# Optimization experiments

Hardware: AMD Instinct MI355X
Metric: run time of the kernel (lower is better)

Reference implementation:

```python
import jax, jax.numpy as jnp
import numpy as np

N_NODES = 100000
N_EDGES = 800000
IN_DIM = 64
HID = 96
OUT_DIM = 1
N_LAYERS = 3
N_CENTRAL = 512
BN_EPS = 1e-5


def setup_inputs() -> dict:
    key = jax.random.key(0)
    ks = jax.random.split(key, 16)
    s = 0.1  # weight scale to keep activations tame
    return {
        "x": jax.random.normal(ks[0], (N_NODES, IN_DIM), jnp.float32),
        "edge_index": jax.random.randint(ks[1], (2, N_EDGES), 0, N_NODES, jnp.int64 if jax.config.jax_enable_x64 else jnp.int32),
        "batch": jnp.zeros((N_NODES,), jnp.int32),
        "central_node_idx": jax.random.randint(ks[2], (N_CENTRAL,), 0, N_NODES, jnp.int32),
        "W_emb": jax.random.normal(ks[3], (IN_DIM, HID), jnp.float32) * s,
        "b_emb": jax.random.normal(ks[4], (HID,), jnp.float32) * s,
        "conv_wl": jax.random.normal(ks[5], (N_LAYERS, HID, HID), jnp.float32) * s,
        "conv_bl": jax.random.normal(ks[6], (N_LAYERS, HID), jnp.float32) * s,
        "conv_wr": jax.random.normal(ks[7], (N_LAYERS, HID, HID), jnp.float32) * s,
        "bn_gamma": jnp.ones((N_LAYERS, HID), jnp.float32),
        "bn_beta": jnp.zeros((N_LAYERS, HID), jnp.float32),
        "W1": jax.random.normal(ks[8], (HID, HID), jnp.float32) * s,
        "b1": jax.random.normal(ks[9], (HID,), jnp.float32) * s,
        "W2": jax.random.normal(ks[10], (HID, OUT_DIM), jnp.float32) * s,
        "b2": jax.random.normal(ks[11], (OUT_DIM,), jnp.float32) * s,
    }


def _sage_mean_agg(h, src, dst, n):
    # PyG SAGEConv mean aggregation: mean of source features at each target node
    msg = h[src]                                             # [E, H] gather
    summed = jax.ops.segment_sum(msg, dst, num_segments=n)   # [N, H] scatter-add
    deg = jax.ops.segment_sum(jnp.ones((src.shape[0],), h.dtype), dst, num_segments=n)
    return summed / jnp.maximum(deg, 1.0)[:, None]


def reference(x, edge_index, batch, central_node_idx, W_emb, b_emb,
              conv_wl, conv_bl, conv_wr, bn_gamma, bn_beta, W1, b1, W2, b2):
    n = x.shape[0]
    src, dst = edge_index[0], edge_index[1]
    h = jax.nn.relu(x @ W_emb + b_emb)                       # [N, H]
    for i in range(conv_wl.shape[0]):
        agg = _sage_mean_agg(h, src, dst, n)
        # SAGEConv: lin_l(agg) (with bias) + lin_r(x_root) (no bias)
        h = agg @ conv_wl[i] + conv_bl[i] + h @ conv_wr[i]
        # BatchNorm1d, training mode: batch stats with biased variance
        mean = h.mean(axis=0)
        var = h.var(axis=0)
        h = (h - mean) * jax.lax.rsqrt(var + BN_EPS) * bn_gamma[i] + bn_beta[i]
        h = jax.nn.relu(h)
    central = h[central_node_idx]                            # [G, H]
    out = jax.nn.relu(central @ W1 + b1) @ W2 + b2           # [G, OUT]
    return out
```

## Files before the change

### kernel.cpp

```cpp
#include <hip/hip_runtime.h>

#define NN 100000
#define NE 800000
#define IND 64
#define HID 96
#define NL 3
#define NC 512
#define BN_EPS 1e-5f

#define NBE ((NN + 127) / 128)
#define NBP (NL * 9)
#define NBF ((NE + 4095) / 4096)
#define NBK2 196
#define BCAP 4864

typedef __attribute__((ext_vector_type(8))) short bf16x8;
typedef __attribute__((ext_vector_type(4))) float f32x4;

static __device__ __forceinline__ float b2f(ushort u) {
    union { uint i; float f; } v; v.i = ((uint)u) << 16; return v.f;
}
static __device__ __forceinline__ ushort f2b(float f) {
    union { float f; uint i; } v; v.f = f;
    uint r = v.i + 0x7FFFu + ((v.i >> 16) & 1u);
    return (ushort)(r >> 16);
}
static __device__ __forceinline__ uint pack2(float a, float b) {
    return (uint)f2b(a) | ((uint)f2b(b) << 16);
}

static __device__ __forceinline__ void prep_one(const float* srcA, const float* srcB,
                                                ushort* dst, int t) {
    int lane = t & 63;
    int ct = (t >> 6) % 6;
    int kt = t / (6 * 64);
    int k0 = kt * 32 + (lane >> 4) * 8;
    int col = ct * 16 + (lane & 15);
    ushort tmp[8];
#pragma unroll
    for (int j = 0; j < 8; ++j) {
        int k = k0 + j;
        const float* src = (srcB == nullptr || k < 96) ? srcA : srcB;
        int kk = (srcB == nullptr || k < 96) ? k : k - 96;
        tmp[j] = f2b(src[kk * HID + col]);
    }
    uint* od = (uint*)(dst + (size_t)t * 8);
    od[0] = (uint)tmp[0] | ((uint)tmp[1] << 16);
    od[1] = (uint)tmp[2] | ((uint)tmp[3] << 16);
    od[2] = (uint)tmp[4] | ((uint)tmp[5] << 16);
    od[3] = (uint)tmp[6] | ((uint)tmp[7] << 16);
}

__global__ __launch_bounds__(256) void k_front(const float* __restrict__ x,
        const float* __restrict__ W_emb, const float* __restrict__ bias,
        ushort* __restrict__ h,
        const float* __restrict__ conv_wl, const float* __restrict__ conv_wr,
        ushort* __restrict__ Bfl, float* __restrict__ stats,
        const int* __restrict__ ei, int* __restrict__ gcur,
        uint* __restrict__ part) {
    __shared__ __align__(16) char smem[24576];
    const int b = blockIdx.x;
    const int tid = threadIdx.x;
    if (b >= NBE) {
        if (b < NBE + NBP) {
            int idx = b - NBE;
            int l = idx / 9, bb = idx % 9;
            int t = bb * 256 + tid;
            if (t < 6 * 6 * 64)
                prep_one(conv_wl + (size_t)l * 9216, conv_wr + (size_t)l * 9216,
                         Bfl + (size_t)l * 18432, t);
            if (bb == 0 && tid < 192) stats[(size_t)l * 192 + tid] = 0.f;
        } else {
            uint* ordbuf = (uint*)smem;
            unsigned char* sbk = (unsigned char*)(smem + 16384);
            int* lhist = (int*)(smem + 20480);
            int* lscan = (int*)(smem + 21504);
            int* lbase = (int*)(smem + 22528);
            int* lcnt2 = (int*)(smem + 23552);
            const int base_e = (b - NBE - NBP) * 4096;
            lhist[tid] = 0; lcnt2[tid] = 0;
            __syncthreads();
#pragma unroll
            for (int it = 0; it < 16; ++it) {
                int e = base_e + it * 256 + tid;
                if (e < NE) atomicAdd(&lhist[ei[NE + e] >> 9], 1);
            }
            __syncthreads();
            int v = lhist[tid];
            lscan[tid] = v;
            __syncthreads();
            for (int off = 1; off < 256; off <<= 1) {
                int t2 = (tid >= off) ? lscan[tid - off] : 0;
                __syncthreads();
                lscan[tid] += t2;
                __syncthreads();
            }
            int excl = lscan[tid] - v;
            __syncthreads();
            lscan[tid] = excl;
            if (v > 0) lbase[tid] = atomicAdd(&gcur[tid], v);
            __syncthreads();
#pragma unroll
            for (int it = 0; it < 16; ++it) {
                int e = base_e + it * 256 + tid;
                if (e < NE) {
                    int s = ei[e], d = ei[NE + e];
                    int bk = d >> 9;
                    int lofs = atomicAdd(&lcnt2[bk], 1);
                    int slot = lscan[bk] + lofs;
                    ordbuf[slot] = (uint)s | ((uint)(d & 511) << 17);
                    sbk[slot] = (unsigned char)bk;
                }
            }
            __syncthreads();
            int total = NE - base_e; if (total > 4096) total = 4096;
            for (int i = tid; i < total; i += 256) {
                int bk = sbk[i];
                part[(size_t)bk * BCAP + lbase[bk] + (i - lscan[bk])] = ordbuf[i];
            }
        }
        return;
    }
    ushort* sB = (ushort*)smem;
    ushort* sT = (ushort*)smem;
    for (int i = tid; i < 768; i += 256) {
        int lane = i & 63;
        int ct = (i >> 6) % 6;
        int kt = i / (6 * 64);
        int k0 = kt * 32 + (lane >> 4) * 8;
        int col = ct * 16 + (lane & 15);
        ushort tmp[8];
#pragma unroll
        for (int j = 0; j < 8; ++j) tmp[j] = f2b(W_emb[(k0 + j) * HID + col]);
        uint4 o;
        o.x = (uint)tmp[0] | ((uint)tmp[1] << 16);
        o.y = (uint)tmp[2] | ((uint)tmp[3] << 16);
        o.z = (uint)tmp[4] | ((uint)tmp[5] << 16);
        o.w = (uint)tmp[6] | ((uint)tmp[7] << 16);
        ((uint4*)sB)[i] = o;
    }
    __syncthreads();
    const int wave = tid >> 6, lane = tid & 63;
    const int rowb = wave * 32;
    const int row0 = b * 128 + rowb;
    const int kof = (lane >> 4) * 8;
    f32x4 acc[2][6];
#pragma unroll
    for (int t = 0; t < 2; ++t)
#pragma unroll
        for (int c = 0; c < 6; ++c) acc[t][c] = (f32x4){0.f, 0.f, 0.f, 0.f};
#pragma unroll
    for (int kt = 0; kt < 2; ++kt) {
        int kk = kt * 32 + kof;
        bf16x8 a[2];
#pragma unroll
        for (int t = 0; t < 2; ++t) {
            int r = row0 + t * 16 + (lane & 15);
            if (r >= NN) r = NN - 1;
            const float* src = x + (size_t)r * IND + kk;
            float4 f0 = *(const float4*)src;
            float4 f1 = *(const float4*)(src + 4);
            a[t][0] = (short)f2b(f0.x); a[t][1] = (short)f2b(f0.y);
            a[t][2] = (short)f2b(f0.z); a[t][3] = (short)f2b(f0.w);
            a[t][4] = (short)f2b(f1.x); a[t][5] = (short)f2b(f1.y);
            a[t][6] = (short)f2b(f1.z); a[t][7] = (short)f2b(f1.w);
        }
#pragma unroll
        for (int ct = 0; ct < 6; ++ct) {
            bf16x8 bb = *(const bf16x8*)&sB[((kt * 6 + ct) * 64 + lane) * 8];
            acc[0][ct] = __builtin_amdgcn_mfma_f32_16x16x32_bf16(a[0], bb, acc[0][ct], 0, 0, 0);
            acc[1][ct] = __builtin_amdgcn_mfma_f32_16x16x32_bf16(a[1], bb, acc[1][ct], 0, 0, 0);
        }
    }
    __syncthreads();
#pragma unroll
    for (int t = 0; t < 2; ++t)
#pragma unroll
        for (int ct = 0; ct < 6; ++ct) {
            int col = ct * 16 + (lane & 15);
            float bv = bias[col];
#pragma unroll
            for (int i = 0; i < 4; ++i) {
                int rb = rowb + t * 16 + (lane >> 4) * 4 + i;
                float v = acc[t][ct][i] + bv;
                sT[rb * HID + col] = f2b(v > 0.f ? v : 0.f);
            }
        }
    __syncthreads();
    for (int i = tid; i < 1536; i += 256) {
        int r = i / 12;
        int g = b * 128 + r;
        if (g < NN) ((uint4*)(h + (size_t)g * HID))[i % 12] = ((uint4*)sT)[i];
    }
}

__global__ __launch_bounds__(256) void k_bscan(const int* __restrict__ gcur,
                                               int* __restrict__ bbase) {
    __shared__ int sd[256];
    const int tid = threadIdx.x;
    int v = (tid < NBK2) ? gcur[tid] : 0;
    sd[tid] = v;
    __syncthreads();
    for (int off = 1; off < 256; off <<= 1) {
        int t = (tid >= off) ? sd[tid - off] : 0;
        __syncthreads();
        sd[tid] += t;
        __syncthreads();
    }
    if (tid < NBK2) bbase[tid] = sd[tid] - v;
}

__global__ __launch_bounds__(256) void k_fill3(const uint* __restrict__ part,
        const int* __restrict__ gcur, const int* __restrict__ bbase,
        int* __restrict__ rp, int* __restrict__ col) {
    __shared__ int lh[512];
    __shared__ int lsc[512];
    __shared__ int pairs[256];
    const int tid = threadIdx.x;
    const int bk = blockIdx.x;
    lh[tid] = 0; lh[tid + 256] = 0;
    __syncthreads();
    const int cnt = gcur[bk];
    const uint* pb = part + (size_t)bk * BCAP;
    for (int e = tid; e < cnt; e += 256) atomicAdd(&lh[pb[e] >> 17], 1);
    __syncthreads();
    int p0 = lh[2 * tid], p1 = lh[2 * tid + 1];
    int ps = p0 + p1;
    pairs[tid] = ps;
    __syncthreads();
    for (int off = 1; off < 256; off <<= 1) {
        int t = (tid >= off) ? pairs[tid - off] : 0;
        __syncthreads();
        pairs[tid] += t;
        __syncthreads();
    }
    int base = bbase[bk];
    int excl = base + pairs[tid] - ps;
    lsc[2 * tid] = excl;
    lsc[2 * tid + 1] = excl + p0;
    __syncthreads();
    const int n0 = bk * 512;
    for (int i = tid; i < 512; i += 256) {
        int n = n0 + i;
        if (n < NN) rp[n] = lsc[i];
    }
    if (bk == NBK2 - 1 && tid == 0) rp[NN] = NE;
    __syncthreads();
    for (int e = tid; e < cnt; e += 256) {
        uint v = pb[e];
        int pos = atomicAdd(&lsc[v >> 17], 1);
        col[pos] = (int)(v & 0x1FFFF);
    }
}

__global__ __launch_bounds__(256, 8) void k_agg(const ushort* __restrict__ pre,
        const int* __restrict__ rp, const int* __restrict__ col,
        const float* __restrict__ stats, const float* __restrict__ gamma,
        const float* __restrict__ beta, ushort* __restrict__ agg) {
    __shared__ float sc[96], sh[96];
    const int tid = threadIdx.x;
    if (tid < 96) {
        float scv = 1.f, shv = 0.f;
        if (stats) {
            float mean = stats[tid] * (1.f / NN);
            float var  = stats[96 + tid] * (1.f / NN) - mean * mean;
            float s = gamma[tid] * rsqrtf(var + BN_EPS);
            scv = s; shv = beta[tid] - mean * s;
        }
        sc[tid] = scv; sh[tid] = shv;
    }
    __syncthreads();
    const int lane = tid & 15;
    const int n = blockIdx.x * 16 + (tid >> 4);
    if (n >= NN) return;
    const float s0a = sc[2*lane],      h0a = sh[2*lane];
    const float s0b = sc[2*lane + 1],  h0b = sh[2*lane + 1];
    const float s1a = sc[2*lane + 32], h1a = sh[2*lane + 32];
    const float s1b = sc[2*lane + 33], h1b = sh[2*lane + 33];
    const float s2a = sc[2*lane + 64], h2a = sh[2*lane + 64];
    const float s2b = sc[2*lane + 65], h2b = sh[2*lane + 65];
    const int e0 = rp[n], e1 = rp[n + 1];
    float a0 = 0.f, a1 = 0.f, a2 = 0.f, a3 = 0.f, a4 = 0.f, a5 = 0.f;
    const uint* hb = (const uint*)pre + lane;
    int e = e0;
    for (; e + 4 <= e1; e += 4) {
        uint u[4][3];
#pragma unroll
        for (int i = 0; i < 4; ++i) {
            const uint* r = hb + (size_t)col[e + i] * 48;
            u[i][0] = r[0]; u[i][1] = r[16]; u[i][2] = r[32];
        }
#pragma unroll
        for (int i = 0; i < 4; ++i) {
            a0 += fmaxf(b2f((ushort)u[i][0])         * s0a + h0a, 0.f);
            a1 += fmaxf(b2f((ushort)(u[i][0] >> 16)) * s0b + h0b, 0.f);
            a2 += fmaxf(b2f((ushort)u[i][1])         * s1a + h1a, 0.f);
            a3 += fmaxf(b2f((ushort)(u[i][1] >> 16)) * s1b + h1b, 0.f);
            a4 += fmaxf(b2f((ushort)u[i][2])         * s2a + h2a, 0.f);
            a5 += fmaxf(b2f((ushort)(u[i][2] >> 16)) * s2b + h2b, 0.f);
        }
    }
    for (; e < e1; ++e) {
        const uint* r = hb + (size_t)col[e] * 48;
        uint u0 = r[0], u1 = r[16], u2 = r[32];
        a0 += fmaxf(b2f((ushort)u0)         * s0a + h0a, 0.f);
        a1 += fmaxf(b2f((ushort)(u0 >> 16)) * s0b + h0b, 0.f);
        a2 += fmaxf(b2f((ushort)u1)         * s1a + h1a, 0.f);
        a3 += fmaxf(b2f((ushort)(u1 >> 16)) * s1b + h1b, 0.f);
        a4 += fmaxf(b2f((ushort)u2)         * s2a + h2a, 0.f);
        a5 += fmaxf(b2f((ushort)(u2 >> 16)) * s2b + h2b, 0.f);
    }
    int d = e1 - e0; if (d < 1) d = 1;
    float inv = 1.0f / (float)d;
    uint* ar = (uint*)agg + (size_t)n * 48 + lane;
    ar[0]  = pack2(a0 * inv, a1 * inv);
    ar[16] = pack2(a2 * inv, a3 * inv);
    ar[32] = pack2(a4 * inv, a5 * inv);
}

__global__ __launch_bounds__(256, 4) void k_gemm(const ushort* __restrict__ aggb,
        const ushort* __restrict__ pre, const ushort* __restrict__ Bf,
        const float* __restrict__ bl, ushort* __restrict__ hnew,
        float* __restrict__ stats,
        const float* __restrict__ statsP, const float* __restrict__ gammaP,
        const float* __restrict__ betaP) {
    __shared__ __align__(16) char smem[40704];
    ushort* sB = (ushort*)smem;
    ushort* sT = (ushort*)smem;
    float*  sredS = (float*)(smem + 36864);
    float*  sredQ = (float*)(smem + 38400);
    float2* sscsh = (float2*)(smem + 39936);
    const int tid = threadIdx.x;
    for (int i = tid; i < 2304; i += 256) ((uint4*)sB)[i] = ((const uint4*)Bf)[i];
    if (tid < 96) {
        float scv = 1.f, shv = 0.f;
        if (statsP) {
            float mean = statsP[tid] * (1.f / NN);
            float var  = statsP[96 + tid] * (1.f / NN) - mean * mean;
            float s = gammaP[tid] * rsqrtf(var + BN_EPS);
            scv = s; shv = betaP[tid] - mean * s;
        }
        sscsh[tid] = make_float2(scv, shv);
    }
    __syncthreads();
    const int wave = tid >> 6, lane = tid & 63;
    const int rowb = wave * 32;
    const int row0 = blockIdx.x * 128 + rowb;
    const int kof = (lane >> 4) * 8;
    f32x4 acc[2][6];
#pragma unroll
    for (int t = 0; t < 2; ++t)
#pragma unroll
        for (int c = 0; c < 6; ++c) acc[t][c] = (f32x4){0.f, 0.f, 0.f, 0.f};
#pragma unroll
    for (int kt = 0; kt < 6; ++kt) {
        bf16x8 a[2];
#pragma unroll
        for (int t = 0; t < 2; ++t) {
            int r = row0 + t * 16 + (lane & 15);
            if (r >= NN) r = NN - 1;
            if (kt < 3) {
                int kk = kt * 32 + kof;
                a[t] = *(const bf16x8*)(aggb + (size_t)r * HID + kk);
            } else {
                int kk = (kt - 3) * 32 + kof;
                bf16x8 raw = *(const bf16x8*)(pre + (size_t)r * HID + kk);
                union { bf16x8 h; uint u[4]; } pk;
#pragma unroll
                for (int j = 0; j < 4; ++j) {
                    float2 p0 = sscsh[kk + 2*j];
                    float2 p1 = sscsh[kk + 2*j + 1];
                    float v0 = fmaxf(b2f((ushort)raw[2*j])     * p0.x + p0.y, 0.f);
                    float v1 = fmaxf(b2f((ushort)raw[2*j + 1]) * p1.x + p1.y, 0.f);
                    pk.u[j] = pack2(v0, v1);
                }
                a[t] = pk.h;
            }
        }
#pragma unroll
        for (int ct = 0; ct < 6; ++ct) {
            bf16x8 bb = *(const bf16x8*)&sB[((kt * 6 + ct) * 64 + lane) * 8];
            acc[0][ct] = __builtin_amdgcn_mfma_f32_16x16x32_bf16(a[0], bb, acc[0][ct], 0, 0, 0);
            acc[1][ct] = __builtin_amdgcn_mfma_f32_16x16x32_bf16(a[1], bb, acc[1][ct], 0, 0, 0);
        }
    }
    __syncthreads();
    float s[6], q[6];
#pragma unroll
    for (int c = 0; c < 6; ++c) { s[c] = 0.f; q[c] = 0.f; }
#pragma unroll
    for (int t = 0; t < 2; ++t)
#pragma unroll
        for (int ct = 0; ct < 6; ++ct) {
            int col = ct * 16 + (lane & 15);
            float bv = bl[col];
#pragma unroll
            for (int i = 0; i < 4; ++i) {
                int rb = rowb + t * 16 + (lane >> 4) * 4 + i;
                int g = blockIdx.x * 128 + rb;
                float v = acc[t][ct][i] + bv;
                if (g < NN) { s[ct] += v; q[ct] += v * v; }
                sT[rb * HID + col] = f2b(v);
            }
        }
#pragma unroll
    for (int c = 0; c < 6; ++c) {
        s[c] += __shfl_xor(s[c], 16); s[c] += __shfl_xor(s[c], 32);
        q[c] += __shfl_xor(q[c], 16); q[c] += __shfl_xor(q[c], 32);
    }
    if (lane < 16) {
#pragma unroll
        for (int c = 0; c < 6; ++c) {
            sredS[wave * 96 + c * 16 + lane] = s[c];
            sredQ[wave * 96 + c * 16 + lane] = q[c];
        }
    }
    __syncthreads();
    if (tid < 96) {
        float S = sredS[tid] + sredS[96 + tid] + sredS[192 + tid] + sredS[288 + tid];
        float Q = sredQ[tid] + sredQ[96 + tid] + sredQ[192 + tid] + sredQ[288 + tid];
        atomicAdd(&stats[tid], S);
        atomicAdd(&stats[96 + tid], Q);
    }
    for (int i = tid; i < 1536; i += 256) {
        int r = i / 12;
        int g = blockIdx.x * 128 + r;
        if (g < NN) ((uint4*)(hnew + (size_t)g * HID))[i % 12] = ((uint4*)sT)[i];
    }
}

__global__ __launch_bounds__(128) void k_mlp(const ushort* __restrict__ pre,
        const int* __restrict__ cidx, const float* __restrict__ stats,
        const float* __restrict__ gamma, const float* __restrict__ beta,
        const float* __restrict__ W1, const float* __restrict__ b1,
        const float* __restrict__ W2, const float* __restrict__ b2,
        float* __restrict__ out) {
    __shared__ float nh[96];
    __shared__ float hid[96];
    __shared__ float red[128];
    const int c = blockIdx.x;
    const int node = cidx[c];
    const int tid = threadIdx.x;
    if (tid < 96) {
        float mean = stats[tid] * (1.f / NN);
        float var  = stats[96 + tid] * (1.f / NN) - mean * mean;
        float s = gamma[tid] * rsqrtf(var + BN_EPS);
        float v = b2f(pre[(size_t)node * 96 + tid]) * s + (beta[tid] - mean * s);
        nh[tid] = fmaxf(v, 0.f);
    }
    __syncthreads();
    if (tid < 96) {
        float a = 0.f;
        for (int k = 0; k < 96; ++k) a += nh[k] * W1[k * 96 + tid];
        hid[tid] = fmaxf(a + b1[tid], 0.f);
    }
    __syncthreads();
    red[tid] = (tid < 96) ? hid[tid] * W2[tid] : 0.f;
    __syncthreads();
    for (int off = 64; off > 0; off >>= 1) {
        if (tid < off) red[tid] += red[tid + off];
        __syncthreads();
    }
    if (tid == 0) out[c] = red[0] + b2[0];
}

extern "C" void kernel_launch(void* const* d_in, const int* in_sizes, int n_in,
                              void* d_out, int out_size, void* d_ws, size_t ws_size,
                              hipStream_t stream) {
    const float* x        = (const float*)d_in[0];
    const int*   ei       = (const int*)d_in[1];
    const int*   cidx     = (const int*)d_in[3];
    const float* W_emb    = (const float*)d_in[4];
    const float* b_emb    = (const float*)d_in[5];
    const float* conv_wl  = (const float*)d_in[6];
    const float* conv_bl  = (const float*)d_in[7];
    const float* conv_wr  = (const float*)d_in[8];
    const float* bn_gamma = (const float*)d_in[9];
    const float* bn_beta  = (const float*)d_in[10];
    const float* W1       = (const float*)d_in[11];
    const float* b1       = (const float*)d_in[12];
    const float* W2       = (const float*)d_in[13];
    const float* b2       = (const float*)d_in[14];
    float* out = (float*)d_out;

    char* ws = (char*)d_ws;
    size_t off = 0;
    auto alloc = [&](size_t bytes) -> void* {
        void* p = ws + off;
        off = (off + bytes + 255) & ~(size_t)255;
        return p;
    };
    ushort* h    = (ushort*)alloc((size_t)NN * 96 * 2);
    ushort* hnew = (ushort*)alloc((size_t)NN * 96 * 2);
    ushort* agg  = (ushort*)alloc((size_t)NN * 96 * 2);
    int*   gcur  = (int*)alloc(256 * 4);
    int*   bbase = (int*)alloc(256 * 4);
    int*   rp    = (int*)alloc((size_t)(NN + 1) * 4);
    int*   col   = (int*)alloc((size_t)NE * 4);
    uint*  part  = (uint*)alloc((size_t)NBK2 * BCAP * 4);
    float* stats = (float*)alloc((size_t)NL * 192 * 4);
    ushort* Bfl  = (ushort*)alloc((size_t)NL * 6 * 6 * 64 * 8 * 2);
    (void)ws_size; (void)in_sizes; (void)n_in; (void)out_size;

    hipMemsetAsync(gcur, 0, 256 * 4, stream);

    k_front<<<NBE + NBP + NBF, 256, 0, stream>>>(x, W_emb, b_emb, h,
        conv_wl, conv_wr, Bfl, stats, ei, gcur, part);
    k_bscan<<<1, 256, 0, stream>>>(gcur, bbase);
    k_fill3<<<NBK2, 256, 0, stream>>>(part, gcur, bbase, rp, col);

    const ushort* src = h;
    ushort* dst = hnew;
    for (int l = 0; l < NL; ++l) {
        const float* stP = (l == 0) ? nullptr : stats + (size_t)(l - 1) * 192;
        const float* gP  = (l == 0) ? nullptr : bn_gamma + (size_t)(l - 1) * 96;
        const float* bP  = (l == 0) ? nullptr : bn_beta + (size_t)(l - 1) * 96;
        k_agg<<<(NN + 15) / 16, 256, 0, stream>>>(src, rp, col, stP, gP, bP, agg);
        k_gemm<<<(NN + 127) / 128, 256, 0, stream>>>(agg, src,
            Bfl + (size_t)l * 18432, conv_bl + (size_t)l * 96, dst,
            stats + (size_t)l * 192, stP, gP, bP);
        const ushort* t = src; src = dst; dst = (ushort*)t;
    }
    k_mlp<<<NC, 128, 0, stream>>>(src, cidx, stats + (size_t)(NL - 1) * 192,
        bn_gamma + (size_t)(NL - 1) * 96, bn_beta + (size_t)(NL - 1) * 96,
        W1, b1, W2, b2, out);
}
```

Measured before the change: 243.9 us.

## Fold bucket scan into fill kernel, stage x in LDS, read GEMM weights from global

Removes the single-block k_bscan launch by having every k_fill3 block redundantly scan the bucket counts itself. In k_front, the x tile is staged as bf16 in LDS with coalesced float4 loads instead of strided per-lane global reads. k_gemm no longer copies weight fragments into LDS: it reads them directly from global/L2, shrinks shared memory and raises the occupancy hint from 4 to 5. The trade-offs are redundant scan work per block and possibly slower B-fragment loads from global.

After: 249.3 us. 1.02x slower.

```diff
diff --git a/kernel.cpp b/kernel.cpp
--- a/kernel.cpp
+++ b/kernel.cpp
@@ -58,7 +58,7 @@
         ushort* __restrict__ Bfl, float* __restrict__ stats,
         const int* __restrict__ ei, int* __restrict__ gcur,
         uint* __restrict__ part) {
-    __shared__ __align__(16) char smem[24576];
+    __shared__ __align__(16) char smem[30720];
     const int b = blockIdx.x;
     const int tid = threadIdx.x;
     if (b >= NBE) {
@@ -122,6 +122,7 @@
         return;
     }
     ushort* sB = (ushort*)smem;
+    ushort* sX = (ushort*)(smem + 12288);
     ushort* sT = (ushort*)smem;
     for (int i = tid; i < 768; i += 256) {
         int lane = i & 63;
@@ -139,10 +140,15 @@
         o.w = (uint)tmp[6] | ((uint)tmp[7] << 16);
         ((uint4*)sB)[i] = o;
     }
+    for (int i = tid; i < 2048; i += 256) {
+        int r = i >> 4, c4 = (i & 15) * 4;
+        int g = b * 128 + r; if (g >= NN) g = NN - 1;
+        float4 f = *(const float4*)&x[(size_t)g * IND + c4];
+        *(uint2*)&sX[r * 72 + c4] = make_uint2(pack2(f.x, f.y), pack2(f.z, f.w));
+    }
     __syncthreads();
     const int wave = tid >> 6, lane = tid & 63;
     const int rowb = wave * 32;
-    const int row0 = b * 128 + rowb;
     const int kof = (lane >> 4) * 8;
     f32x4 acc[2][6];
 #pragma unroll
@@ -155,15 +161,8 @@
         bf16x8 a[2];
 #pragma unroll
         for (int t = 0; t < 2; ++t) {
-            int r = row0 + t * 16 + (lane & 15);
-            if (r >= NN) r = NN - 1;
-            const float* src = x + (size_t)r * IND + kk;
-            float4 f0 = *(const float4*)src;
-            float4 f1 = *(const float4*)(src + 4);
-            a[t][0] = (short)f2b(f0.x); a[t][1] = (short)f2b(f0.y);
-            a[t][2] = (short)f2b(f0.z); a[t][3] = (short)f2b(f0.w);
-            a[t][4] = (short)f2b(f1.x); a[t][5] = (short)f2b(f1.y);
-            a[t][6] = (short)f2b(f1.z); a[t][7] = (short)f2b(f1.w);
+            int rb = rowb + t * 16 + (lane & 15);
+            a[t] = *(const bf16x8*)&sX[rb * 72 + kk];
         }
 #pragma unroll
         for (int ct = 0; ct < 6; ++ct) {
@@ -194,32 +193,29 @@
     }
 }
 
-__global__ __launch_bounds__(256) void k_bscan(const int* __restrict__ gcur,
-                                               int* __restrict__ bbase) {
-    __shared__ int sd[256];
-    const int tid = threadIdx.x;
-    int v = (tid < NBK2) ? gcur[tid] : 0;
-    sd[tid] = v;
-    __syncthreads();
-    for (int off = 1; off < 256; off <<= 1) {
-        int t = (tid >= off) ? sd[tid - off] : 0;
-        __syncthreads();
-        sd[tid] += t;
-        __syncthreads();
-    }
-    if (tid < NBK2) bbase[tid] = sd[tid] - v;
-}
-
 __global__ __launch_bounds__(256) void k_fill3(const uint* __restrict__ part,
-        const int* __restrict__ gcur, const int* __restrict__ bbase,
-        int* __restrict__ rp, int* __restrict__ col) {
+        const int* __restrict__ gcur, int* __restrict__ rp, int* __restrict__ col) {
     __shared__ int lh[512];
     __shared__ int lsc[512];
     __shared__ int pairs[256];
+    __shared__ int sge[256];
     const int tid = threadIdx.x;
     const int bk = blockIdx.x;
+    int gv = (tid < NBK2) ? gcur[tid] : 0;
+    sge[tid] = gv;
     lh[tid] = 0; lh[tid + 256] = 0;
     __syncthreads();
+    for (int off = 1; off < 256; off <<= 1) {
+        int t = (tid >= off) ? sge[tid - off] : 0;
+        __syncthreads();
+        sge[tid] += t;
+        __syncthreads();
+    }
+    int incl = sge[tid];
+    __syncthreads();
+    sge[tid] = incl - gv;
+    __syncthreads();
+    const int base = sge[bk];
     const int cnt = gcur[bk];
     const uint* pb = part + (size_t)bk * BCAP;
     for (int e = tid; e < cnt; e += 256) atomicAdd(&lh[pb[e] >> 17], 1);
@@ -234,7 +230,6 @@
         pairs[tid] += t;
         __syncthreads();
     }
-    int base = bbase[bk];
     int excl = base + pairs[tid] - ps;
     lsc[2 * tid] = excl;
     lsc[2 * tid + 1] = excl + p0;
@@ -318,20 +313,18 @@
     ar[32] = pack2(a4 * inv, a5 * inv);
 }
 
-__global__ __launch_bounds__(256, 4) void k_gemm(const ushort* __restrict__ aggb,
+__global__ __launch_bounds__(256, 5) void k_gemm(const ushort* __restrict__ aggb,
         const ushort* __restrict__ pre, const ushort* __restrict__ Bf,
         const float* __restrict__ bl, ushort* __restrict__ hnew,
         float* __restrict__ stats,
         const float* __restrict__ statsP, const float* __restrict__ gammaP,
         const float* __restrict__ betaP) {
-    __shared__ __align__(16) char smem[40704];
-    ushort* sB = (ushort*)smem;
+    __shared__ __align__(16) char smem[28416];
     ushort* sT = (ushort*)smem;
-    float*  sredS = (float*)(smem + 36864);
-    float*  sredQ = (float*)(smem + 38400);
-    float2* sscsh = (float2*)(smem + 39936);
+    float*  sredS = (float*)(smem + 24576);
+    float*  sredQ = (float*)(smem + 26112);
+    float2* sscsh = (float2*)(smem + 27648);
     const int tid = threadIdx.x;
-    for (int i = tid; i < 2304; i += 256) ((uint4*)sB)[i] = ((const uint4*)Bf)[i];
     if (tid < 96) {
         float scv = 1.f, shv = 0.f;
         if (statsP) {
@@ -379,12 +372,11 @@
         }
 #pragma unroll
         for (int ct = 0; ct < 6; ++ct) {
-            bf16x8 bb = *(const bf16x8*)&sB[((kt * 6 + ct) * 64 + lane) * 8];
+            bf16x8 bb = *(const bf16x8*)&Bf[((kt * 6 + ct) * 64 + lane) * 8];
             acc[0][ct] = __builtin_amdgcn_mfma_f32_16x16x32_bf16(a[0], bb, acc[0][ct], 0, 0, 0);
             acc[1][ct] = __builtin_amdgcn_mfma_f32_16x16x32_bf16(a[1], bb, acc[1][ct], 0, 0, 0);
         }
     }
-    __syncthreads();
     float s[6], q[6];
 #pragma unroll
     for (int c = 0; c < 6; ++c) { s[c] = 0.f; q[c] = 0.f; }
@@ -494,7 +486,6 @@
     ushort* hnew = (ushort*)alloc((size_t)NN * 96 * 2);
     ushort* agg  = (ushort*)alloc((size_t)NN * 96 * 2);
     int*   gcur  = (int*)alloc(256 * 4);
-    int*   bbase = (int*)alloc(256 * 4);
     int*   rp    = (int*)alloc((size_t)(NN + 1) * 4);
     int*   col   = (int*)alloc((size_t)NE * 4);
     uint*  part  = (uint*)alloc((size_t)NBK2 * BCAP * 4);
@@ -506,8 +497,7 @@
 
     k_front<<<NBE + NBP + NBF, 256, 0, stream>>>(x, W_emb, b_emb, h,
         conv_wl, conv_wr, Bfl, stats, ei, gcur, part);
-    k_bscan<<<1, 256, 0, stream>>>(gcur, bbase);
-    k_fill3<<<NBK2, 256, 0, stream>>>(part, gcur, bbase, rp, col);
+    k_fill3<<<NBK2, 256, 0, stream>>>(part, gcur, rp, col);
 
     const ushort* src = h;
     ushort* dst = hnew;
```
